# Kernel optimization log

Hardware: AMD Instinct MI355X
Metric: run time of the kernel (lower is better)

Reference implementation:

```python
import jax, jax.numpy as jnp
import numpy as np

EPSILON = 1e-36


def setup_inputs() -> dict:
    key = jax.random.key(0)
    k1, k2, k3, k4 = jax.random.split(key, 4)
    n, in_dim, out_dim = 8192, 128, 128
    x = jax.random.normal(k1, (n, in_dim), dtype=jnp.float32)
    # xavier-uniform-like scale for W_real
    limit = float(np.sqrt(6.0 / (in_dim + out_dim)))
    W_real = jax.random.uniform(k2, (in_dim, out_dim), dtype=jnp.float32, minval=-limit, maxval=limit)
    W_imag = jax.random.uniform(k3, (in_dim, out_dim), dtype=jnp.float32, minval=-0.1, maxval=0.1)
    G = jax.random.uniform(k4, (in_dim, out_dim), dtype=jnp.float32, minval=0.0, maxval=1.0)
    return {"x": x, "W_real": W_real, "W_imag": W_imag, "G": G}


def reference(x, W_real, W_imag, G):
    Gc = jnp.clip(G, 0.0, 1.0)                                   # (i,o)
    # R: (n,i,o) = |x| gated toward 1 by (1-G)
    R = (jnp.abs(x) + EPSILON)[:, :, None] * Gc[None] + (1.0 - Gc)[None]
    # K: pi where x<0, gated by G
    K = jnp.pi * (x < 0).astype(x.dtype)[:, :, None] * Gc[None]  # (n,i,o)
    logR = jnp.log(R)
    A = jnp.einsum('nio,io->no', logR, W_real) - jnp.einsum('nio,io->no', K, W_imag)
    B = jnp.einsum('nio,io->no', logR, W_imag) + jnp.einsum('nio,io->no', K, W_real)
    return jnp.exp(A) * jnp.cos(B)
```

## Files before the change

### kernel.cpp

```cpp
#include <hip/hip_runtime.h>
#include <math.h>


#define NROWS 8192
#define DIM   128
#define RPB   8
#define NT    512
#define IQ    32
#define PI_F  3.14159265358979323846f
#define LN2_F 0.69314718055994530942f

typedef float v2f __attribute__((ext_vector_type(2)));

static __device__ __forceinline__ v2f vfma2(v2f a, v2f b, v2f c) {
    return __builtin_elementwise_fma(a, b, c);
}

__global__ __launch_bounds__(256) void prep_w(
    const float* __restrict__ Wr, const float* __restrict__ Wi,
    const float* __restrict__ G, float4* __restrict__ wq)
{
    int t = blockIdx.x * 256 + threadIdx.x;
    if (t < DIM * DIM) {
        float g  = fminf(fmaxf(G[t], 0.0f), 1.0f);
        wq[t] = make_float4(LN2_F * Wr[t], LN2_F * Wi[t], g, g * (1.0f / LN2_F));
    }
}

template <bool PACKED>
__global__ __launch_bounds__(NT, 8) void main_kernel(
    const float* __restrict__ x, const float4* __restrict__ wq,
    const float* __restrict__ Wr, const float* __restrict__ Wi,
    const float* __restrict__ G, float* __restrict__ out)
{
    __shared__ float sbuf[4 * RPB * DIM];
    float* am1p = sbuf;
    float* psp  = sbuf + DIM * RPB;

    const int tid   = threadIdx.x;
    const int o     = tid & (DIM - 1);
    const int q     = tid >> 7;
    const int nbase = blockIdx.x * RPB;
    const float* xb = x + (size_t)nbase * DIM;

    {
        float2 v = ((const float2*)xb)[tid];
        int e = tid * 2;
        int i = e & (DIM - 1), r = e >> 7;
        am1p[i * RPB + r]       = fabsf(v.x) - 1.0f;
        am1p[(i + 1) * RPB + r] = fabsf(v.y) - 1.0f;
        psp[i * RPB + r]        = (v.x < 0.0f) ? PI_F : 0.0f;
        psp[(i + 1) * RPB + r]  = (v.y < 0.0f) ? PI_F : 0.0f;
    }
    __syncthreads();

    v2f accA[4], accB[4];
#pragma unroll
    for (int p = 0; p < 4; ++p) { accA[p] = (v2f){0.f, 0.f}; accB[p] = (v2f){0.f, 0.f}; }

    const int ibase = q * IQ;
#pragma unroll 2
    for (int ii = 0; ii < IQ; ++ii) {
        const int i = ibase + ii;
        float wrl, wil, g, gq;
        if (PACKED) {
            float4 w = wq[i * DIM + o];
            wrl = w.x; wil = w.y; g = w.z; gq = w.w;
        } else {
            g   = fminf(fmaxf(G[i * DIM + o], 0.0f), 1.0f);
            wrl = LN2_F * Wr[i * DIM + o];
            wil = LN2_F * Wi[i * DIM + o];
            gq  = g * (1.0f / LN2_F);
        }
        const float ngwi = -gq * wil;
        const float gwr  =  gq * wrl;
        const v2f gg2   = {g, g};
        const v2f wrl2  = {wrl, wrl};
        const v2f wil2  = {wil, wil};
        const v2f ngwi2 = {ngwi, ngwi};
        const v2f gwr2  = {gwr, gwr};
        const v2f one2  = {1.0f, 1.0f};

        const float4* a4 = (const float4*)(am1p + i * RPB);
        const float4* p4 = (const float4*)(psp  + i * RPB);
        float4 a03 = a4[0], a47 = a4[1];
        float4 s03 = p4[0], s47 = p4[1];

#define ROWPAIR(mx, my, sx, sy, idx)                                        \
        do {                                                                \
            v2f t2 = vfma2((v2f){mx, my}, gg2, one2);                       \
            v2f l2 = { __log2f(t2.x), __log2f(t2.y) };                      \
            v2f s2 = {sx, sy};                                              \
            accA[idx] = vfma2(l2, wrl2, vfma2(s2, ngwi2, accA[idx]));       \
            accB[idx] = vfma2(l2, wil2, vfma2(s2, gwr2,  accB[idx]));       \
        } while (0)

        ROWPAIR(a03.x, a03.y, s03.x, s03.y, 0);
        ROWPAIR(a03.z, a03.w, s03.z, s03.w, 1);
        ROWPAIR(a47.x, a47.y, s47.x, s47.y, 2);
        ROWPAIR(a47.z, a47.w, s47.z, s47.w, 3);
#undef ROWPAIR
    }

    float* pP = sbuf;
    const int c = tid * 2;
    const int r = c >> 7, oo = c & (DIM - 1);

    __syncthreads();
#pragma unroll
    for (int p = 0; p < 4; ++p) {
        pP[q * (RPB * DIM) + (2 * p) * DIM + o]     = accA[p].x;
        pP[q * (RPB * DIM) + (2 * p + 1) * DIM + o] = accA[p].y;
    }
    __syncthreads();
    v2f A = {0.f, 0.f};
#pragma unroll
    for (int qq = 0; qq < 4; ++qq)
        A += *(const v2f*)&pP[qq * (RPB * DIM) + r * DIM + oo];
    __syncthreads();
#pragma unroll
    for (int p = 0; p < 4; ++p) {
        pP[q * (RPB * DIM) + (2 * p) * DIM + o]     = accB[p].x;
        pP[q * (RPB * DIM) + (2 * p + 1) * DIM + o] = accB[p].y;
    }
    __syncthreads();
    v2f B = {0.f, 0.f};
#pragma unroll
    for (int qq = 0; qq < 4; ++qq)
        B += *(const v2f*)&pP[qq * (RPB * DIM) + r * DIM + oo];

    float2 res;
    res.x = __expf(A.x) * __cosf(B.x);
    res.y = __expf(A.y) * __cosf(B.y);
    *(float2*)&out[(size_t)(nbase + r) * DIM + oo] = res;
}

extern "C" void kernel_launch(void* const* d_in, const int* in_sizes, int n_in,
                              void* d_out, int out_size, void* d_ws, size_t ws_size,
                              hipStream_t stream) {
    const float* x  = (const float*)d_in[0];
    const float* Wr = (const float*)d_in[1];
    const float* Wi = (const float*)d_in[2];
    const float* G  = (const float*)d_in[3];
    float* out = (float*)d_out;

    const size_t wq_bytes = (size_t)DIM * DIM * sizeof(float4);
    if (ws_size >= wq_bytes) {
        float4* wq = (float4*)d_ws;
        prep_w<<<(DIM * DIM + 255) / 256, 256, 0, stream>>>(Wr, Wi, G, wq);
        main_kernel<true><<<NROWS / RPB, NT, 0, stream>>>(x, wq,
                                                          nullptr, nullptr, nullptr, out);
    } else {
        main_kernel<false><<<NROWS / RPB, NT, 0, stream>>>(x, nullptr,
                                                           Wr, Wi, G, out);
    }
}
```

Measured before the change: 85.44 us.

## Give each thread two output columns and split the input dim eight ways

Each thread now covers two output columns (o and o+64) over 16 input indices, instead of one column over 32. The 512 threads are split into eight groups along the input dimension, and shared memory is doubled so the eight-way partial-sum reduction fits. The per-row LDS loads of |x|-1 and the sign term are reused across both columns, which halves shared-memory reads per FMA. The cost is more accumulator registers and a larger cross-group reduction. The per-element log2 count is unchanged, so the change only helps if LDS traffic, not the transcendental unit, is the limit.

```diff
diff --git a/kernel.cpp b/kernel.cpp
--- a/kernel.cpp
+++ b/kernel.cpp
@@ -6,7 +6,7 @@
 #define DIM   128
 #define RPB   8
 #define NT    512
-#define IQ    32
+#define IQ    16
 #define PI_F  3.14159265358979323846f
 #define LN2_F 0.69314718055994530942f
 
@@ -33,13 +33,13 @@
     const float* __restrict__ Wr, const float* __restrict__ Wi,
     const float* __restrict__ G, float* __restrict__ out)
 {
-    __shared__ float sbuf[4 * RPB * DIM];
+    __shared__ float sbuf[8 * RPB * DIM];
     float* am1p = sbuf;
     float* psp  = sbuf + DIM * RPB;
 
     const int tid   = threadIdx.x;
-    const int o     = tid & (DIM - 1);
-    const int q     = tid >> 7;
+    const int o64   = tid & 63;
+    const int q     = tid >> 6;
     const int nbase = blockIdx.x * RPB;
     const float* xb = x + (size_t)nbase * DIM;
 
@@ -54,52 +54,65 @@
     }
     __syncthreads();
 
-    v2f accA[4], accB[4];
+    v2f aA0[4], aB0[4], aA1[4], aB1[4];
 #pragma unroll
-    for (int p = 0; p < 4; ++p) { accA[p] = (v2f){0.f, 0.f}; accB[p] = (v2f){0.f, 0.f}; }
+    for (int p = 0; p < 4; ++p) {
+        aA0[p] = (v2f){0.f, 0.f}; aB0[p] = (v2f){0.f, 0.f};
+        aA1[p] = (v2f){0.f, 0.f}; aB1[p] = (v2f){0.f, 0.f};
+    }
 
     const int ibase = q * IQ;
 #pragma unroll 2
     for (int ii = 0; ii < IQ; ++ii) {
         const int i = ibase + ii;
-        float wrl, wil, g, gq;
+        float wrl0, wil0, g0, gq0, wrl1, wil1, g1, gq1;
         if (PACKED) {
-            float4 w = wq[i * DIM + o];
-            wrl = w.x; wil = w.y; g = w.z; gq = w.w;
+            float4 w0 = wq[i * DIM + o64];
+            float4 w1 = wq[i * DIM + o64 + 64];
+            wrl0 = w0.x; wil0 = w0.y; g0 = w0.z; gq0 = w0.w;
+            wrl1 = w1.x; wil1 = w1.y; g1 = w1.z; gq1 = w1.w;
         } else {
-            g   = fminf(fmaxf(G[i * DIM + o], 0.0f), 1.0f);
-            wrl = LN2_F * Wr[i * DIM + o];
-            wil = LN2_F * Wi[i * DIM + o];
-            gq  = g * (1.0f / LN2_F);
+            g0   = fminf(fmaxf(G[i * DIM + o64], 0.0f), 1.0f);
+            wrl0 = LN2_F * Wr[i * DIM + o64];
+            wil0 = LN2_F * Wi[i * DIM + o64];
+            gq0  = g0 * (1.0f / LN2_F);
+            g1   = fminf(fmaxf(G[i * DIM + o64 + 64], 0.0f), 1.0f);
+            wrl1 = LN2_F * Wr[i * DIM + o64 + 64];
+            wil1 = LN2_F * Wi[i * DIM + o64 + 64];
+            gq1  = g1 * (1.0f / LN2_F);
         }
-        const float ngwi = -gq * wil;
-        const float gwr  =  gq * wrl;
-        const v2f gg2   = {g, g};
-        const v2f wrl2  = {wrl, wrl};
-        const v2f wil2  = {wil, wil};
-        const v2f ngwi2 = {ngwi, ngwi};
-        const v2f gwr2  = {gwr, gwr};
-        const v2f one2  = {1.0f, 1.0f};
+        const float ngwi0 = -gq0 * wil0, gwr0 = gq0 * wrl0;
+        const float ngwi1 = -gq1 * wil1, gwr1 = gq1 * wrl1;
 
         const float4* a4 = (const float4*)(am1p + i * RPB);
         const float4* p4 = (const float4*)(psp  + i * RPB);
-        float4 a03 = a4[0], a47 = a4[1];
-        float4 s03 = p4[0], s47 = p4[1];
 
-#define ROWPAIR(mx, my, sx, sy, idx)                                        \
+#define RP(mx, my, sx, sy, g_, wrl_, wil_, ngwi_, gwr_, accA, accB)         \
         do {                                                                \
-            v2f t2 = vfma2((v2f){mx, my}, gg2, one2);                       \
+            v2f t2 = vfma2((v2f){mx, my}, (v2f){g_, g_}, (v2f){1.f, 1.f});  \
             v2f l2 = { __log2f(t2.x), __log2f(t2.y) };                      \
             v2f s2 = {sx, sy};                                              \
-            accA[idx] = vfma2(l2, wrl2, vfma2(s2, ngwi2, accA[idx]));       \
-            accB[idx] = vfma2(l2, wil2, vfma2(s2, gwr2,  accB[idx]));       \
+            accA = vfma2(l2, (v2f){wrl_, wrl_},                             \
+                         vfma2(s2, (v2f){ngwi_, ngwi_}, accA));             \
+            accB = vfma2(l2, (v2f){wil_, wil_},                             \
+                         vfma2(s2, (v2f){gwr_, gwr_},  accB));              \
         } while (0)
 
-        ROWPAIR(a03.x, a03.y, s03.x, s03.y, 0);
-        ROWPAIR(a03.z, a03.w, s03.z, s03.w, 1);
-        ROWPAIR(a47.x, a47.y, s47.x, s47.y, 2);
-        ROWPAIR(a47.z, a47.w, s47.z, s47.w, 3);
-#undef ROWPAIR
+        {
+            float4 a = a4[0], s = p4[0];
+            RP(a.x, a.y, s.x, s.y, g0, wrl0, wil0, ngwi0, gwr0, aA0[0], aB0[0]);
+            RP(a.z, a.w, s.z, s.w, g0, wrl0, wil0, ngwi0, gwr0, aA0[1], aB0[1]);
+            RP(a.x, a.y, s.x, s.y, g1, wrl1, wil1, ngwi1, gwr1, aA1[0], aB1[0]);
+            RP(a.z, a.w, s.z, s.w, g1, wrl1, wil1, ngwi1, gwr1, aA1[1], aB1[1]);
+        }
+        {
+            float4 a = a4[1], s = p4[1];
+            RP(a.x, a.y, s.x, s.y, g0, wrl0, wil0, ngwi0, gwr0, aA0[2], aB0[2]);
+            RP(a.z, a.w, s.z, s.w, g0, wrl0, wil0, ngwi0, gwr0, aA0[3], aB0[3]);
+            RP(a.x, a.y, s.x, s.y, g1, wrl1, wil1, ngwi1, gwr1, aA1[2], aB1[2]);
+            RP(a.z, a.w, s.z, s.w, g1, wrl1, wil1, ngwi1, gwr1, aA1[3], aB1[3]);
+        }
+#undef RP
     }
 
     float* pP = sbuf;
@@ -109,24 +122,28 @@
     __syncthreads();
 #pragma unroll
     for (int p = 0; p < 4; ++p) {
-        pP[q * (RPB * DIM) + (2 * p) * DIM + o]     = accA[p].x;
-        pP[q * (RPB * DIM) + (2 * p + 1) * DIM + o] = accA[p].y;
+        pP[q * (RPB * DIM) + (2 * p) * DIM + o64]          = aA0[p].x;
+        pP[q * (RPB * DIM) + (2 * p + 1) * DIM + o64]      = aA0[p].y;
+        pP[q * (RPB * DIM) + (2 * p) * DIM + o64 + 64]     = aA1[p].x;
+        pP[q * (RPB * DIM) + (2 * p + 1) * DIM + o64 + 64] = aA1[p].y;
     }
     __syncthreads();
     v2f A = {0.f, 0.f};
 #pragma unroll
-    for (int qq = 0; qq < 4; ++qq)
+    for (int qq = 0; qq < 8; ++qq)
         A += *(const v2f*)&pP[qq * (RPB * DIM) + r * DIM + oo];
     __syncthreads();
 #pragma unroll
     for (int p = 0; p < 4; ++p) {
-        pP[q * (RPB * DIM) + (2 * p) * DIM + o]     = accB[p].x;
-        pP[q * (RPB * DIM) + (2 * p + 1) * DIM + o] = accB[p].y;
+        pP[q * (RPB * DIM) + (2 * p) * DIM + o64]          = aB0[p].x;
+        pP[q * (RPB * DIM) + (2 * p + 1) * DIM + o64]      = aB0[p].y;
+        pP[q * (RPB * DIM) + (2 * p) * DIM + o64 + 64]     = aB1[p].x;
+        pP[q * (RPB * DIM) + (2 * p + 1) * DIM + o64 + 64] = aB1[p].y;
     }
     __syncthreads();
     v2f B = {0.f, 0.f};
 #pragma unroll
-    for (int qq = 0; qq < 4; ++qq)
+    for (int qq = 0; qq < 8; ++qq)
         B += *(const v2f*)&pP[qq * (RPB * DIM) + r * DIM + oo];
 
     float2 res;
```

Result: slower. 89.61 us (+4.9%).
